# Kernel optimization log

Measured on AMD Instinct MI355X. Metric: run time of the kernel, lower is better.

The kernel has to match this reference:

```python
import jax, jax.numpy as jnp
import numpy as np
from jax import lax

T, D, HID, C = 16384, 1024, 1024, 16
H = HID // 2  # per-direction hidden size


def _uniform(key, shape, bound):
    return jax.random.uniform(key, shape, jnp.float32, -bound, bound)


def setup_inputs() -> dict:
    key = jax.random.key(0)
    ks = jax.random.split(key, 16)
    s = 1.0 / np.sqrt(H)        # PyTorch LSTM init bound
    sl = 1.0 / np.sqrt(HID)     # PyTorch Linear init bound
    return {
        "sequence": jax.random.normal(ks[0], (T, D), jnp.float32),
        "h0": jax.random.normal(ks[1], (2, 1, H), jnp.float32),
        "c0": jax.random.normal(ks[2], (2, 1, H), jnp.float32),
        "w_ih_f": _uniform(ks[3], (4 * H, D), s),
        "w_hh_f": _uniform(ks[4], (4 * H, H), s),
        "b_ih_f": _uniform(ks[5], (4 * H,), s),
        "b_hh_f": _uniform(ks[6], (4 * H,), s),
        "w_ih_b": _uniform(ks[7], (4 * H, D), s),
        "w_hh_b": _uniform(ks[8], (4 * H, H), s),
        "b_ih_b": _uniform(ks[9], (4 * H,), s),
        "b_hh_b": _uniform(ks[10], (4 * H,), s),
        "w_lin": _uniform(ks[11], (C, HID), sl),
        "b_lin": _uniform(ks[12], (C,), sl),
        "transitions": jax.random.uniform(ks[13], (C, C), jnp.float32),  # torch.rand
    }


def _lstm_scan(x, h0, c0, w_ih, w_hh, b_ih, b_hh, reverse):
    # x: [T, D]; PyTorch gate order: i, f, g, o
    def step(carry, xt):
        h, c = carry
        g = w_ih @ xt + b_ih + w_hh @ h + b_hh  # [4H]
        i, f, gg, o = jnp.split(g, 4)
        i = jax.nn.sigmoid(i)
        f = jax.nn.sigmoid(f)
        gg = jnp.tanh(gg)
        o = jax.nn.sigmoid(o)
        c = f * c + i * gg
        h = o * jnp.tanh(c)
        return (h, c), h
    _, hs = lax.scan(step, (h0, c0), x, reverse=reverse)
    return hs  # [T, H], hs[t] = hidden at time t (aligned for both directions)


def _viterbi(feats, transitions):
    # feats: [T, C]; init forward_var = zeros (per the original torch.full(..., 0))
    def vstep(fv, feat):
        scores = fv[None, :] + transitions          # [C_next, C_prev]
        bp = jnp.argmax(scores, axis=1)             # backpointers
        fv2 = jnp.max(scores, axis=1) + feat
        return fv2, bp
    fv, bps = lax.scan(vstep, jnp.zeros((C,), feats.dtype), feats)
    best = jnp.argmax(fv)
    path_score = fv[best]
    def bstep(b, bp_row):
        nb = bp_row[b]
        return nb, nb
    _, rev = lax.scan(bstep, best, bps, reverse=True)  # rev[t] = state before step t's transition
    best_path = jnp.concatenate([rev, best[None]])     # length T+1, matches torch output
    return path_score, best_path


def reference(sequence, h0, c0, w_ih_f, w_hh_f, b_ih_f, b_hh_f,
              w_ih_b, w_hh_b, b_ih_b, b_hh_b, w_lin, b_lin, transitions):
    hs_f = _lstm_scan(sequence, h0[0, 0], c0[0, 0], w_ih_f, w_hh_f, b_ih_f, b_hh_f, False)
    hs_b = _lstm_scan(sequence, h0[1, 0], c0[1, 0], w_ih_b, w_hh_b, b_ih_b, b_hh_b, True)
    lstm_out = jnp.concatenate([hs_f, hs_b], axis=-1)   # [T, HID]
    feats = lstm_out @ w_lin.T + b_lin                  # [T, C]
    return _viterbi(feats, transitions)
```

## Files before the change

kernel.cpp:

```cpp
#include <hip/hip_runtime.h>

#define T_STEPS 16384
#define TC      8192
#define DMODEL  1024
#define HID     512
#define G4      2048
#define NC      16

static const unsigned long long OFF_ZF    = 0ull;
static const unsigned long long OFF_ZB    = 16777216ull;
static const unsigned long long OFF_HF    = 33554432ull;
static const unsigned long long OFF_HB    = 41943040ull;
static const unsigned long long OFF_FEATS = 50331648ull;
static const unsigned long long OFF_CST   = 50593792ull;
static const unsigned long long FLOATS_TOTAL = 50594816ull;
static const unsigned long long OFF_BP_B = FLOATS_TOTAL * 4ull;
static const unsigned long long OFF_P_B  = OFF_BP_B + 262144ull;
static const unsigned long long OFF_EX_B = OFF_P_B + 262144ull;
static const unsigned long long OFF_BT_B = OFF_EX_B + 16384ull;
static const unsigned long long NEED_B   = OFF_BT_B + 64ull;

__global__ __launch_bounds__(256) void zgemm_kernel(
    const float* __restrict__ X,
    const float* __restrict__ W0, const float* __restrict__ bi0,
    const float* __restrict__ bh0, float* __restrict__ Z0, int t00,
    const float* __restrict__ W1, const float* __restrict__ bi1,
    const float* __restrict__ bh1, float* __restrict__ Z1, int t01)
{
    const int dir = blockIdx.z;
    const float* W  = dir ? W1 : W0;
    const float* bi = dir ? bi1 : bi0;
    const float* bh = dir ? bh1 : bh0;
    float* Z        = dir ? Z1 : Z0;
    const int t0    = dir ? t01 : t00;

    const int m0 = blockIdx.y * 64;
    const int n0 = blockIdx.x * 64;

    __shared__ __align__(16) float As[16][68];
    __shared__ __align__(16) float Bs[16][68];

    const int tid = threadIdx.x;
    const int lr = tid >> 2;
    const int ls = tid & 3;
    const int tx = tid & 15;
    const int ty = tid >> 4;

    float acc[4][4] = {};

    for (int k0 = 0; k0 < DMODEL; k0 += 16) {
        float4 av = *(const float4*)&X[(unsigned long long)(t0 + m0 + lr) * DMODEL + k0 + ls * 4];
        float4 bv = *(const float4*)&W[(unsigned long long)(n0 + lr) * DMODEL + k0 + ls * 4];
        __syncthreads();
        As[ls*4+0][lr] = av.x; As[ls*4+1][lr] = av.y; As[ls*4+2][lr] = av.z; As[ls*4+3][lr] = av.w;
        Bs[ls*4+0][lr] = bv.x; Bs[ls*4+1][lr] = bv.y; Bs[ls*4+2][lr] = bv.z; Bs[ls*4+3][lr] = bv.w;
        __syncthreads();
        #pragma unroll
        for (int k = 0; k < 16; ++k) {
            float4 a = *(const float4*)&As[k][ty * 4];
            float4 b = *(const float4*)&Bs[k][tx * 4];
            acc[0][0] += a.x*b.x; acc[0][1] += a.x*b.y; acc[0][2] += a.x*b.z; acc[0][3] += a.x*b.w;
            acc[1][0] += a.y*b.x; acc[1][1] += a.y*b.y; acc[1][2] += a.y*b.z; acc[1][3] += a.y*b.w;
            acc[2][0] += a.z*b.x; acc[2][1] += a.z*b.y; acc[2][2] += a.z*b.z; acc[2][3] += a.z*b.w;
            acc[3][0] += a.w*b.x; acc[3][1] += a.w*b.y; acc[3][2] += a.w*b.z; acc[3][3] += a.w*b.w;
        }
    }
    float4 bi4 = *(const float4*)&bi[n0 + tx * 4];
    float4 bh4 = *(const float4*)&bh[n0 + tx * 4];
    float bx = bi4.x + bh4.x, by = bi4.y + bh4.y, bz = bi4.z + bh4.z, bw = bi4.w + bh4.w;
    #pragma unroll
    for (int i = 0; i < 4; ++i) {
        float4 o;
        o.x = acc[i][0] + bx; o.y = acc[i][1] + by; o.z = acc[i][2] + bz; o.w = acc[i][3] + bw;
        *(float4*)&Z[(unsigned long long)(m0 + ty * 4 + i) * G4 + n0 + tx * 4] = o;
    }
}

__global__ __launch_bounds__(256, 1) void recur_kernel(
    const float* __restrict__ Zf, const float* __restrict__ Zb,
    const float* __restrict__ whh_f, const float* __restrict__ whh_b,
    const float* __restrict__ h0, const float* __restrict__ c0,
    float* __restrict__ hf, float* __restrict__ hb,
    unsigned long long* __restrict__ exf, unsigned long long* __restrict__ exb,
    float* __restrict__ c_state, int s0, int zf_t0, int zb_t0)
{
    const int wg  = blockIdx.x;
    const int dir = wg >> 5;
    const int g   = wg & 31;
    const float* Z   = dir ? Zb : Zf;
    const float* whh = dir ? whh_b : whh_f;
    float* hout      = dir ? hb : hf;
    const int zt0    = dir ? zb_t0 : zf_t0;
    unsigned long long* ex = dir ? exb : exf;

    const int tid  = threadIdx.x;
    const int w    = tid >> 6;
    const int lane = tid & 63;
    const int G    = lane >> 4;
    const int u    = lane & 15;
    const int R    = 512 * G + 16 * g + u;

    float wreg[128];
    {
        const float* src = &whh[(unsigned long long)R * HID + w * 128];
        #pragma unroll
        for (int j4 = 0; j4 < 32; ++j4) {
            float4 v = *(const float4*)&src[j4 * 4];
            wreg[j4*4+0] = v.x; wreg[j4*4+1] = v.y; wreg[j4*4+2] = v.z; wreg[j4*4+3] = v.w;
        }
    }

    __shared__ __align__(16) float h_lds[512];
    __shared__ __align__(16) float p_lds[256];

    float cst = 0.0f;
    if (w == 0 && lane < 16)
        cst = (s0 == 0) ? c0[dir * HID + 16 * g + lane]
                        : c_state[dir * HID + 16 * g + lane];

    for (int s = s0; s < s0 + TC; ++s) {
        const int t = dir ? (T_STEPS - 1 - s) : s;
        float zr = 0.0f;
        if (w == 0) zr = Z[(unsigned long long)(t - zt0) * G4 + R];

        int dead = 0;
        if (s == 0) {
            h_lds[2*tid]   = h0[dir * HID + 2*tid];
            h_lds[2*tid+1] = h0[dir * HID + 2*tid + 1];
        } else {
            const int par = s & 1;
            const unsigned long long want = (unsigned long long)s;
            #pragma unroll
            for (int r = 0; r < 2; ++r) {
                const int idx = 2 * tid + r;
                unsigned long long v;
                int guard = 0;
                do {
                    v = __hip_atomic_load(&ex[par * 512 + idx], __ATOMIC_RELAXED,
                                          __HIP_MEMORY_SCOPE_AGENT);
                    if (++guard >= (1 << 17)) { dead = 1; break; }
                } while ((v >> 32) != want);
                union { unsigned int ui; float f; } cv;
                cv.ui = (unsigned int)v;
                h_lds[idx] = cv.f;
            }
        }
        if (__syncthreads_or(dead)) break;

        float acc = 0.0f;
        const float4* h4 = (const float4*)&h_lds[w * 128];
        #pragma unroll
        for (int c4 = 0; c4 < 32; ++c4) {
            float4 hv = h4[c4];
            acc += wreg[c4*4+0]*hv.x + wreg[c4*4+1]*hv.y
                 + wreg[c4*4+2]*hv.z + wreg[c4*4+3]*hv.w;
        }
        p_lds[tid] = acc;
        __syncthreads();

        if (w == 0) {
            float rv = p_lds[lane] + p_lds[64+lane] + p_lds[128+lane] + p_lds[192+lane] + zr;
            float iv = __shfl(rv, u,      64);
            float fv = __shfl(rv, u + 16, 64);
            float gv = __shfl(rv, u + 32, 64);
            float ov = __shfl(rv, u + 48, 64);
            if (lane < 16) {
                float ig = 1.0f / (1.0f + expf(-iv));
                float fg = 1.0f / (1.0f + expf(-fv));
                float gg = tanhf(gv);
                float og = 1.0f / (1.0f + expf(-ov));
                float cn = fg * cst + ig * gg;
                float hn = og * tanhf(cn);
                cst = cn;
                hout[(unsigned long long)t * HID + 16 * g + lane] = hn;
                union { float f; unsigned int ui; } cv; cv.f = hn;
                unsigned long long pv = ((unsigned long long)(s + 1) << 32) | (unsigned long long)cv.ui;
                __hip_atomic_store(&ex[((s + 1) & 1) * 512 + 16 * g + lane], pv,
                                   __ATOMIC_RELAXED, __HIP_MEMORY_SCOPE_AGENT);
            }
        }
        __syncthreads();
    }

    if (w == 0 && lane < 16)
        c_state[dir * HID + 16 * g + lane] = cst;
}

__global__ __launch_bounds__(256) void feats_kernel(
    const float* __restrict__ hf, const float* __restrict__ hb,
    const float* __restrict__ wlin, const float* __restrict__ blin,
    float* __restrict__ feats)
{
    const int t = blockIdx.x;
    __shared__ __align__(16) float hl[1024];
    const int tid = threadIdx.x;
    {
        const float* src = (tid < 128) ? &hf[(unsigned long long)t * HID + tid * 4]
                                       : &hb[(unsigned long long)t * HID + (tid - 128) * 4];
        *(float4*)&hl[tid * 4] = *(const float4*)src;
    }
    __syncthreads();
    const int c = tid >> 4, p = tid & 15;
    float s = 0.0f;
    #pragma unroll
    for (int j = 0; j < 16; ++j) {
        float4 h4 = *(const float4*)&hl[p * 4 + j * 64];
        float4 w4 = *(const float4*)&wlin[(unsigned long long)c * 1024 + p * 4 + j * 64];
        s += h4.x*w4.x + h4.y*w4.y + h4.z*w4.z + h4.w*w4.w;
    }
    s += __shfl_down(s, 8, 16);
    s += __shfl_down(s, 4, 16);
    s += __shfl_down(s, 2, 16);
    s += __shfl_down(s, 1, 16);
    if (p == 0) feats[t * NC + c] = s + blin[c];
}

__global__ __launch_bounds__(64) void viterbi_kernel(
    const float* __restrict__ feats, const float* __restrict__ trans,
    unsigned char* __restrict__ bp, float* __restrict__ out,
    unsigned int* __restrict__ bT)
{
    __shared__ __align__(16) float fl[4096];
    __shared__ __align__(16) float fvs[16];
    const int l = threadIdx.x;
    float tr[16];
    if (l < 16) {
        #pragma unroll
        for (int j = 0; j < 16; ++j) tr[j] = trans[l * 16 + j];
    }
    float fv = 0.0f;
    for (int cb = 0; cb < 64; ++cb) {
        #pragma unroll
        for (int j = 0; j < 16; ++j)
            *(float4*)&fl[j * 256 + l * 4] =
                *(const float4*)&feats[cb * 4096 + j * 256 + l * 4];
        __syncthreads();
        if (l < 16) {
            for (int k = 0; k < 256; ++k) {
                float m = __shfl(fv, 0, 16) + tr[0];
                int bi = 0;
                #pragma unroll
                for (int j = 1; j < 16; ++j) {
                    float sc = __shfl(fv, j, 16) + tr[j];
                    if (sc > m) { m = sc; bi = j; }
                }
                bp[(unsigned long long)(cb * 256 + k) * 16 + l] = (unsigned char)bi;
                fv = m + fl[k * 16 + l];
            }
        }
        __syncthreads();
    }
    if (l < 16) fvs[l] = fv;
    __syncthreads();
    if (l == 0) {
        float best = fvs[0]; int bi = 0;
        #pragma unroll
        for (int j = 1; j < 16; ++j) if (fvs[j] > best) { best = fvs[j]; bi = j; }
        out[0] = best;
        out[1 + T_STEPS] = (float)bi;
        *bT = (unsigned int)bi;
    }
}

__global__ __launch_bounds__(64) void maps_kernel(
    const unsigned char* __restrict__ bp, unsigned char* __restrict__ P)
{
    const int j = blockIdx.x;
    const int l = threadIdx.x;
    __shared__ __align__(16) unsigned char lb[4096];
    __shared__ __align__(16) unsigned char lp[4096];
    #pragma unroll
    for (int i = 0; i < 4; ++i)
        *(uint4*)&lb[i * 1024 + l * 16] = *(const uint4*)&bp[(unsigned long long)j * 4096 + i * 1024 + l * 16];
    __syncthreads();
    if (l < 16) {
        int cur = l;
        for (int k = 255; k >= 0; --k) {
            cur = lb[k * 16 + cur];
            lp[k * 16 + l] = (unsigned char)cur;
        }
    }
    __syncthreads();
    #pragma unroll
    for (int i = 0; i < 4; ++i)
        *(uint4*)&P[(unsigned long long)j * 4096 + i * 1024 + l * 16] = *(const uint4*)&lp[i * 1024 + l * 16];
}

__global__ __launch_bounds__(64) void path_kernel(
    const unsigned char* __restrict__ P, const unsigned int* __restrict__ bT,
    float* __restrict__ out)
{
    const int j = blockIdx.x;
    const int l = threadIdx.x;
    int e = (int)(*bT);
    for (int i = 63; i > j; --i) e = P[(unsigned long long)i * 4096 + e];
    for (int k = l; k < 256; k += 64)
        out[1 + j * 256 + k] = (float)P[(unsigned long long)j * 4096 + k * 16 + e];
}

__global__ void fb_kernel(float* out, int n, float v0) {
    int i = blockIdx.x * 256 + threadIdx.x;
    if (i < n) out[i] = (i == 0) ? v0 : 0.0f;
}

extern "C" void kernel_launch(void* const* d_in, const int* in_sizes, int n_in,
                              void* d_out, int out_size, void* d_ws, size_t ws_size,
                              hipStream_t stream) {
    const float* seq   = (const float*)d_in[0];
    const float* h0    = (const float*)d_in[1];
    const float* c0    = (const float*)d_in[2];
    const float* wih_f = (const float*)d_in[3];
    const float* whh_f = (const float*)d_in[4];
    const float* bih_f = (const float*)d_in[5];
    const float* bhh_f = (const float*)d_in[6];
    const float* wih_b = (const float*)d_in[7];
    const float* whh_b = (const float*)d_in[8];
    const float* bih_b = (const float*)d_in[9];
    const float* bhh_b = (const float*)d_in[10];
    const float* wlin  = (const float*)d_in[11];
    const float* blin  = (const float*)d_in[12];
    const float* trans = (const float*)d_in[13];
    float* out = (float*)d_out;

    if (ws_size < NEED_B) {
        fb_kernel<<<(out_size + 255) / 256, 256, 0, stream>>>(out, out_size, -(float)ws_size);
        return;
    }

    float* wsf = (float*)d_ws;
    float* Zf    = wsf + OFF_ZF;
    float* Zb    = wsf + OFF_ZB;
    float* hf    = wsf + OFF_HF;
    float* hb    = wsf + OFF_HB;
    float* feats = wsf + OFF_FEATS;
    float* cstate= wsf + OFF_CST;
    unsigned char* bp = (unsigned char*)d_ws + OFF_BP_B;
    unsigned char* P  = (unsigned char*)d_ws + OFF_P_B;
    unsigned long long* exf = (unsigned long long*)((char*)d_ws + OFF_EX_B);
    unsigned long long* exb = exf + 1024;
    unsigned int* bT = (unsigned int*)((char*)d_ws + OFF_BT_B);

    hipMemsetAsync((void*)exf, 0, 16384, stream);

    for (int ci = 0; ci < 2; ++ci) {
        int s0    = ci * TC;
        int zf_t0 = ci * TC;
        int zb_t0 = T_STEPS - (ci + 1) * TC;

        zgemm_kernel<<<dim3(32, TC / 64, 2), 256, 0, stream>>>(
            seq, wih_f, bih_f, bhh_f, Zf, zf_t0, wih_b, bih_b, bhh_b, Zb, zb_t0);

        void* args[] = { (void*)&Zf, (void*)&Zb, (void*)&whh_f, (void*)&whh_b,
                         (void*)&h0, (void*)&c0, (void*)&hf, (void*)&hb,
                         (void*)&exf, (void*)&exb, (void*)&cstate,
                         (void*)&s0, (void*)&zf_t0, (void*)&zb_t0 };
        hipError_t e = hipLaunchCooperativeKernel(
            reinterpret_cast<void*>(recur_kernel), dim3(64), dim3(256),
            args, 0, stream);
        if (e != hipSuccess) {
            recur_kernel<<<64, 256, 0, stream>>>(Zf, Zb, whh_f, whh_b, h0, c0,
                                                 hf, hb, exf, exb, cstate,
                                                 s0, zf_t0, zb_t0);
        }
    }

    feats_kernel<<<16384, 256, 0, stream>>>(hf, hb, wlin, blin, feats);
    viterbi_kernel<<<1, 64, 0, stream>>>(feats, trans, bp, out, bT);
    maps_kernel<<<64, 64, 0, stream>>>(bp, P);
    path_kernel<<<64, 64, 0, stream>>>(P, bT, out);
}
```

Baseline: 47.75 ms.

## Fuse input-projection GEMM and LSTM recurrence into one persistent producer-consumer kernel

Merges the input-projection GEMM and the recurrent LSTM kernel into one cooperative launch of 256 blocks. 64 blocks run the recurrence while 192 blocks compute Z in 1024-step chunks into a double buffer, with counters signalling when each chunk is ready or consumed. This hides the GEMM time behind the latency-bound recurrence and shrinks the Z workspace. The recurrence also double-buffers the partial-sum LDS to drop one barrier per step and computes the gate activations across all 64 lanes before the shuffles. The risks are contention between GEMM blocks and recurrence blocks for memory bandwidth, and spin-wait deadlocks that are only escaped through guard counters.

```diff
diff --git a/kernel.cpp b/kernel.cpp
--- a/kernel.cpp
+++ b/kernel.cpp
@@ -1,189 +1,214 @@
 #include <hip/hip_runtime.h>
 
 #define T_STEPS 16384
-#define TC      8192
+#define CSTEPS  1024
+#define NCHUNK  16
 #define DMODEL  1024
 #define HID     512
 #define G4      2048
 #define NC      16
-
-static const unsigned long long OFF_ZF    = 0ull;
-static const unsigned long long OFF_ZB    = 16777216ull;
-static const unsigned long long OFF_HF    = 33554432ull;
-static const unsigned long long OFF_HB    = 41943040ull;
-static const unsigned long long OFF_FEATS = 50331648ull;
-static const unsigned long long OFF_CST   = 50593792ull;
-static const unsigned long long FLOATS_TOTAL = 50594816ull;
-static const unsigned long long OFF_BP_B = FLOATS_TOTAL * 4ull;
-static const unsigned long long OFF_P_B  = OFF_BP_B + 262144ull;
-static const unsigned long long OFF_EX_B = OFF_P_B + 262144ull;
-static const unsigned long long OFF_BT_B = OFF_EX_B + 16384ull;
-static const unsigned long long NEED_B   = OFF_BT_B + 64ull;
-
-__global__ __launch_bounds__(256) void zgemm_kernel(
-    const float* __restrict__ X,
-    const float* __restrict__ W0, const float* __restrict__ bi0,
-    const float* __restrict__ bh0, float* __restrict__ Z0, int t00,
-    const float* __restrict__ W1, const float* __restrict__ bi1,
-    const float* __restrict__ bh1, float* __restrict__ Z1, int t01)
-{
-    const int dir = blockIdx.z;
-    const float* W  = dir ? W1 : W0;
-    const float* bi = dir ? bi1 : bi0;
-    const float* bh = dir ? bh1 : bh0;
-    float* Z        = dir ? Z1 : Z0;
-    const int t0    = dir ? t01 : t00;
-
-    const int m0 = blockIdx.y * 64;
-    const int n0 = blockIdx.x * 64;
-
-    __shared__ __align__(16) float As[16][68];
-    __shared__ __align__(16) float Bs[16][68];
-
-    const int tid = threadIdx.x;
-    const int lr = tid >> 2;
-    const int ls = tid & 3;
-    const int tx = tid & 15;
-    const int ty = tid >> 4;
-
-    float acc[4][4] = {};
-
-    for (int k0 = 0; k0 < DMODEL; k0 += 16) {
-        float4 av = *(const float4*)&X[(unsigned long long)(t0 + m0 + lr) * DMODEL + k0 + ls * 4];
-        float4 bv = *(const float4*)&W[(unsigned long long)(n0 + lr) * DMODEL + k0 + ls * 4];
-        __syncthreads();
-        As[ls*4+0][lr] = av.x; As[ls*4+1][lr] = av.y; As[ls*4+2][lr] = av.z; As[ls*4+3][lr] = av.w;
-        Bs[ls*4+0][lr] = bv.x; Bs[ls*4+1][lr] = bv.y; Bs[ls*4+2][lr] = bv.z; Bs[ls*4+3][lr] = bv.w;
-        __syncthreads();
-        #pragma unroll
-        for (int k = 0; k < 16; ++k) {
-            float4 a = *(const float4*)&As[k][ty * 4];
-            float4 b = *(const float4*)&Bs[k][tx * 4];
-            acc[0][0] += a.x*b.x; acc[0][1] += a.x*b.y; acc[0][2] += a.x*b.z; acc[0][3] += a.x*b.w;
-            acc[1][0] += a.y*b.x; acc[1][1] += a.y*b.y; acc[1][2] += a.y*b.z; acc[1][3] += a.y*b.w;
-            acc[2][0] += a.z*b.x; acc[2][1] += a.z*b.y; acc[2][2] += a.z*b.z; acc[2][3] += a.z*b.w;
-            acc[3][0] += a.w*b.x; acc[3][1] += a.w*b.y; acc[3][2] += a.w*b.z; acc[3][3] += a.w*b.w;
-        }
-    }
-    float4 bi4 = *(const float4*)&bi[n0 + tx * 4];
-    float4 bh4 = *(const float4*)&bh[n0 + tx * 4];
-    float bx = bi4.x + bh4.x, by = bi4.y + bh4.y, bz = bi4.z + bh4.z, bw = bi4.w + bh4.w;
-    #pragma unroll
-    for (int i = 0; i < 4; ++i) {
-        float4 o;
-        o.x = acc[i][0] + bx; o.y = acc[i][1] + by; o.z = acc[i][2] + bz; o.w = acc[i][3] + bw;
-        *(float4*)&Z[(unsigned long long)(m0 + ty * 4 + i) * G4 + n0 + tx * 4] = o;
-    }
-}
-
-__global__ __launch_bounds__(256, 1) void recur_kernel(
-    const float* __restrict__ Zf, const float* __restrict__ Zb,
+#define NGEMMB  192
+
+static const size_t OFF_Z     = 0;
+static const size_t OFF_HF    = 8388608ull;
+static const size_t OFF_HB    = 16777216ull;
+static const size_t OFF_FEATS = 25165824ull;
+static const size_t FLOATS_TOTAL = 25427968ull;
+static const size_t OFF_BP_B  = FLOATS_TOTAL * 4ull;
+static const size_t OFF_P_B   = OFF_BP_B + 262144ull;
+static const size_t OFF_EX_B  = OFF_P_B + 262144ull;
+static const size_t OFF_CTR_B = OFF_EX_B + 16384ull;
+static const size_t NEED_B    = OFF_CTR_B + 256ull;
+
+__global__ __launch_bounds__(256, 1) void fused_kernel(
+    const float* __restrict__ seq,
+    const float* __restrict__ wih_f, const float* __restrict__ bih_f, const float* __restrict__ bhh_f,
+    const float* __restrict__ wih_b, const float* __restrict__ bih_b, const float* __restrict__ bhh_b,
     const float* __restrict__ whh_f, const float* __restrict__ whh_b,
     const float* __restrict__ h0, const float* __restrict__ c0,
     float* __restrict__ hf, float* __restrict__ hb,
+    float* __restrict__ Zbuf,
     unsigned long long* __restrict__ exf, unsigned long long* __restrict__ exb,
-    float* __restrict__ c_state, int s0, int zf_t0, int zb_t0)
-{
-    const int wg  = blockIdx.x;
-    const int dir = wg >> 5;
-    const int g   = wg & 31;
-    const float* Z   = dir ? Zb : Zf;
-    const float* whh = dir ? whh_b : whh_f;
-    float* hout      = dir ? hb : hf;
-    const int zt0    = dir ? zb_t0 : zf_t0;
-    unsigned long long* ex = dir ? exb : exf;
-
-    const int tid  = threadIdx.x;
-    const int w    = tid >> 6;
-    const int lane = tid & 63;
-    const int G    = lane >> 4;
-    const int u    = lane & 15;
-    const int R    = 512 * G + 16 * g + u;
-
-    float wreg[128];
-    {
-        const float* src = &whh[(unsigned long long)R * HID + w * 128];
-        #pragma unroll
-        for (int j4 = 0; j4 < 32; ++j4) {
-            float4 v = *(const float4*)&src[j4 * 4];
-            wreg[j4*4+0] = v.x; wreg[j4*4+1] = v.y; wreg[j4*4+2] = v.z; wreg[j4*4+3] = v.w;
-        }
-    }
-
-    __shared__ __align__(16) float h_lds[512];
-    __shared__ __align__(16) float p_lds[256];
-
-    float cst = 0.0f;
-    if (w == 0 && lane < 16)
-        cst = (s0 == 0) ? c0[dir * HID + 16 * g + lane]
-                        : c_state[dir * HID + 16 * g + lane];
-
-    for (int s = s0; s < s0 + TC; ++s) {
-        const int t = dir ? (T_STEPS - 1 - s) : s;
-        float zr = 0.0f;
-        if (w == 0) zr = Z[(unsigned long long)(t - zt0) * G4 + R];
+    unsigned int* __restrict__ gemm_done, unsigned int* __restrict__ recur_prog)
+{
+    const int bid = blockIdx.x;
+    const int tid = threadIdx.x;
+
+    if (bid < 64) {
+        const int dir = bid >> 5;
+        const int g   = bid & 31;
+        const float* whh = dir ? whh_b : whh_f;
+        float* hout      = dir ? hb : hf;
+        unsigned long long* ex = dir ? exb : exf;
+
+        const int w = tid >> 6, lane = tid & 63;
+        const int G = lane >> 4, u = lane & 15;
+        const int R = 512 * G + 16 * g + u;
+
+        float wreg[128];
+        {
+            const float* src = &whh[(size_t)R * HID + w * 128];
+            #pragma unroll
+            for (int j = 0; j < 32; ++j) {
+                float4 v = *(const float4*)&src[j * 4];
+                wreg[j*4+0]=v.x; wreg[j*4+1]=v.y; wreg[j*4+2]=v.z; wreg[j*4+3]=v.w;
+            }
+        }
+
+        __shared__ __align__(16) float h_lds[512];
+        __shared__ __align__(16) float p_lds[2][256];
+
+        float cst = 0.f;
+        if (w == 0 && lane < 16) cst = c0[dir * HID + 16 * g + lane];
+
+        {
+            const int i0 = 128 * w + 2 * lane;
+            h_lds[i0]     = h0[dir * HID + i0];
+            h_lds[i0 + 1] = h0[dir * HID + i0 + 1];
+        }
 
         int dead = 0;
-        if (s == 0) {
-            h_lds[2*tid]   = h0[dir * HID + 2*tid];
-            h_lds[2*tid+1] = h0[dir * HID + 2*tid + 1];
-        } else {
+        const float* Zd = Zbuf + (size_t)dir * 2 * CSTEPS * G4;
+
+        for (int s = 0; s < T_STEPS; ++s) {
+            if ((s & (CSTEPS - 1)) == 0) {
+                if (tid == 0) {
+                    const int cg = s >> 10;
+                    int guard = 0; unsigned int gd;
+                    do {
+                        gd = __hip_atomic_load(&gemm_done[cg], __ATOMIC_RELAXED,
+                                               __HIP_MEMORY_SCOPE_AGENT);
+                        if (++guard > (1 << 20)) { dead = 1; break; }
+                    } while (gd < (unsigned)NGEMMB);
+                }
+                if (__syncthreads_or(dead)) break;
+            }
+            const int c   = s >> 10;
             const int par = s & 1;
-            const unsigned long long want = (unsigned long long)s;
-            #pragma unroll
-            for (int r = 0; r < 2; ++r) {
-                const int idx = 2 * tid + r;
-                unsigned long long v;
+            const int t   = dir ? (T_STEPS - 1 - s) : s;
+            const int rr  = dir ? (1023 - (s & 1023)) : (s & 1023);
+
+            float zr = 0.f;
+            if (w == 0)
+                zr = __hip_atomic_load(&Zd[((size_t)(c & 1) * CSTEPS + rr) * G4 + R],
+                                       __ATOMIC_RELAXED, __HIP_MEMORY_SCOPE_AGENT);
+
+            if (s > 0) {
+                const unsigned long long want = (unsigned long long)(unsigned)s;
+                const int i0 = 128 * w + 2 * lane;
+                unsigned long long v0, v1;
                 int guard = 0;
+                for (;;) {
+                    v0 = __hip_atomic_load(&ex[par*512 + i0],     __ATOMIC_RELAXED, __HIP_MEMORY_SCOPE_AGENT);
+                    v1 = __hip_atomic_load(&ex[par*512 + i0 + 1], __ATOMIC_RELAXED, __HIP_MEMORY_SCOPE_AGENT);
+                    if (((v0 >> 32) == want) & ((v1 >> 32) == want)) break;
+                    if (++guard > (1 << 16)) { dead = 1; break; }
+                }
+                union { unsigned int ui; float f; } ca, cb;
+                ca.ui = (unsigned int)v0; cb.ui = (unsigned int)v1;
+                h_lds[i0]     = ca.f;
+                h_lds[i0 + 1] = cb.f;
+            }
+
+            float acc = 0.f;
+            {
+                const float4* h4 = (const float4*)&h_lds[w * 128];
+                #pragma unroll
+                for (int j = 0; j < 32; ++j) {
+                    float4 hv = h4[j];
+                    acc += wreg[j*4+0]*hv.x + wreg[j*4+1]*hv.y
+                         + wreg[j*4+2]*hv.z + wreg[j*4+3]*hv.w;
+                }
+            }
+            p_lds[par][tid] = acc;
+            if (__syncthreads_or(dead)) break;
+
+            if (w == 0) {
+                float rv = p_lds[par][lane] + p_lds[par][64+lane]
+                         + p_lds[par][128+lane] + p_lds[par][192+lane] + zr;
+                float a = (G == 2) ? tanhf(rv) : 1.f / (1.f + expf(-rv));
+                float ig = __shfl(a, u,      64);
+                float fg = __shfl(a, u + 16, 64);
+                float gg = __shfl(a, u + 32, 64);
+                float og = __shfl(a, u + 48, 64);
+                if (lane < 16) {
+                    float cn = fg * cst + ig * gg;
+                    cst = cn;
+                    float hn = og * tanhf(cn);
+                    union { float f; unsigned int ui; } cv; cv.f = hn;
+                    __hip_atomic_store(&ex[((s + 1) & 1) * 512 + 16 * g + lane],
+                        ((unsigned long long)(unsigned)(s + 1) << 32) | (unsigned long long)cv.ui,
+                        __ATOMIC_RELAXED, __HIP_MEMORY_SCOPE_AGENT);
+                    hout[(size_t)t * HID + 16 * g + lane] = hn;
+                }
+                if ((s & (CSTEPS - 1)) == (CSTEPS - 1) && lane == 0)
+                    __hip_atomic_fetch_add(&recur_prog[c], 1u, __ATOMIC_RELAXED,
+                                           __HIP_MEMORY_SCOPE_AGENT);
+            }
+        }
+    } else {
+        const int gb = bid - 64;
+        __shared__ __align__(16) float As[16][68];
+        __shared__ __align__(16) float Bs[16][68];
+        const int lr = tid >> 2, ls = tid & 3, tx = tid & 15, ty = tid >> 4;
+
+        for (int cc = 0; cc < NCHUNK; ++cc) {
+            if (cc >= 2 && tid == 0) {
+                int guard = 0; unsigned int rp;
                 do {
-                    v = __hip_atomic_load(&ex[par * 512 + idx], __ATOMIC_RELAXED,
-                                          __HIP_MEMORY_SCOPE_AGENT);
-                    if (++guard >= (1 << 17)) { dead = 1; break; }
-                } while ((v >> 32) != want);
-                union { unsigned int ui; float f; } cv;
-                cv.ui = (unsigned int)v;
-                h_lds[idx] = cv.f;
-            }
-        }
-        if (__syncthreads_or(dead)) break;
-
-        float acc = 0.0f;
-        const float4* h4 = (const float4*)&h_lds[w * 128];
-        #pragma unroll
-        for (int c4 = 0; c4 < 32; ++c4) {
-            float4 hv = h4[c4];
-            acc += wreg[c4*4+0]*hv.x + wreg[c4*4+1]*hv.y
-                 + wreg[c4*4+2]*hv.z + wreg[c4*4+3]*hv.w;
-        }
-        p_lds[tid] = acc;
-        __syncthreads();
-
-        if (w == 0) {
-            float rv = p_lds[lane] + p_lds[64+lane] + p_lds[128+lane] + p_lds[192+lane] + zr;
-            float iv = __shfl(rv, u,      64);
-            float fv = __shfl(rv, u + 16, 64);
-            float gv = __shfl(rv, u + 32, 64);
-            float ov = __shfl(rv, u + 48, 64);
-            if (lane < 16) {
-                float ig = 1.0f / (1.0f + expf(-iv));
-                float fg = 1.0f / (1.0f + expf(-fv));
-                float gg = tanhf(gv);
-                float og = 1.0f / (1.0f + expf(-ov));
-                float cn = fg * cst + ig * gg;
-                float hn = og * tanhf(cn);
-                cst = cn;
-                hout[(unsigned long long)t * HID + 16 * g + lane] = hn;
-                union { float f; unsigned int ui; } cv; cv.f = hn;
-                unsigned long long pv = ((unsigned long long)(s + 1) << 32) | (unsigned long long)cv.ui;
-                __hip_atomic_store(&ex[((s + 1) & 1) * 512 + 16 * g + lane], pv,
-                                   __ATOMIC_RELAXED, __HIP_MEMORY_SCOPE_AGENT);
-            }
-        }
-        __syncthreads();
-    }
-
-    if (w == 0 && lane < 16)
-        c_state[dir * HID + 16 * g + lane] = cst;
+                    rp = __hip_atomic_load(&recur_prog[cc - 2], __ATOMIC_RELAXED,
+                                           __HIP_MEMORY_SCOPE_AGENT);
+                    if (++guard > (1 << 20)) break;
+                } while (rp < 64u);
+            }
+            __syncthreads();
+
+            for (int tix = gb; tix < 2 * 16 * 32; tix += NGEMMB) {
+                const int dr  = tix >> 9;
+                const int rem = tix & 511;
+                const int mt  = rem >> 5;
+                const int nt  = rem & 31;
+                const int t0  = dr ? (T_STEPS - (cc + 1) * CSTEPS) : (cc * CSTEPS);
+                const float* W  = dr ? wih_b : wih_f;
+                const float* bi = dr ? bih_b : bih_f;
+                const float* bh = dr ? bhh_b : bhh_f;
+                float* Zt = Zbuf + (size_t)(dr * 2 + (cc & 1)) * CSTEPS * G4;
+
+                float acc[4][4] = {};
+                for (int k0 = 0; k0 < DMODEL; k0 += 16) {
+                    float4 av = *(const float4*)&seq[(size_t)(t0 + mt*64 + lr) * DMODEL + k0 + ls*4];
+                    float4 bv = *(const float4*)&W[(size_t)(nt*64 + lr) * DMODEL + k0 + ls*4];
+                    __syncthreads();
+                    As[ls*4+0][lr]=av.x; As[ls*4+1][lr]=av.y; As[ls*4+2][lr]=av.z; As[ls*4+3][lr]=av.w;
+                    Bs[ls*4+0][lr]=bv.x; Bs[ls*4+1][lr]=bv.y; Bs[ls*4+2][lr]=bv.z; Bs[ls*4+3][lr]=bv.w;
+                    __syncthreads();
+                    #pragma unroll
+                    for (int k = 0; k < 16; ++k) {
+                        float4 a = *(const float4*)&As[k][ty * 4];
+                        float4 b = *(const float4*)&Bs[k][tx * 4];
+                        acc[0][0]+=a.x*b.x; acc[0][1]+=a.x*b.y; acc[0][2]+=a.x*b.z; acc[0][3]+=a.x*b.w;
+                        acc[1][0]+=a.y*b.x; acc[1][1]+=a.y*b.y; acc[1][2]+=a.y*b.z; acc[1][3]+=a.y*b.w;
+                        acc[2][0]+=a.z*b.x; acc[2][1]+=a.z*b.y; acc[2][2]+=a.z*b.z; acc[2][3]+=a.z*b.w;
+                        acc[3][0]+=a.w*b.x; acc[3][1]+=a.w*b.y; acc[3][2]+=a.w*b.z; acc[3][3]+=a.w*b.w;
+                    }
+                }
+                float4 b4  = *(const float4*)&bi[nt * 64 + tx * 4];
+                float4 c4v = *(const float4*)&bh[nt * 64 + tx * 4];
+                float bx=b4.x+c4v.x, by=b4.y+c4v.y, bz=b4.z+c4v.z, bw_=b4.w+c4v.w;
+                #pragma unroll
+                for (int i = 0; i < 4; ++i) {
+                    float4 o;
+                    o.x=acc[i][0]+bx; o.y=acc[i][1]+by; o.z=acc[i][2]+bz; o.w=acc[i][3]+bw_;
+                    *(float4*)&Zt[(size_t)(mt*64 + ty*4 + i) * G4 + nt*64 + tx*4] = o;
+                }
+            }
+            __threadfence();
+            __syncthreads();
+            if (tid == 0)
+                __hip_atomic_fetch_add(&gemm_done[cc], 1u, __ATOMIC_RELEASE,
+                                       __HIP_MEMORY_SCOPE_AGENT);
+        }
+    }
 }
 
 __global__ __launch_bounds__(256) void feats_kernel(
@@ -195,8 +220,8 @@
     __shared__ __align__(16) float hl[1024];
     const int tid = threadIdx.x;
     {
-        const float* src = (tid < 128) ? &hf[(unsigned long long)t * HID + tid * 4]
-                                       : &hb[(unsigned long long)t * HID + (tid - 128) * 4];
+        const float* src = (tid < 128) ? &hf[(size_t)t * HID + tid * 4]
+                                       : &hb[(size_t)t * HID + (tid - 128) * 4];
         *(float4*)&hl[tid * 4] = *(const float4*)src;
     }
     __syncthreads();
@@ -205,7 +230,7 @@
     #pragma unroll
     for (int j = 0; j < 16; ++j) {
         float4 h4 = *(const float4*)&hl[p * 4 + j * 64];
-        float4 w4 = *(const float4*)&wlin[(unsigned long long)c * 1024 + p * 4 + j * 64];
+        float4 w4 = *(const float4*)&wlin[(size_t)c * 1024 + p * 4 + j * 64];
         s += h4.x*w4.x + h4.y*w4.y + h4.z*w4.z + h4.w*w4.w;
     }
     s += __shfl_down(s, 8, 16);
@@ -244,7 +269,7 @@
                     float sc = __shfl(fv, j, 16) + tr[j];
                     if (sc > m) { m = sc; bi = j; }
                 }
-                bp[(unsigned long long)(cb * 256 + k) * 16 + l] = (unsigned char)bi;
+                bp[(size_t)(cb * 256 + k) * 16 + l] = (unsigned char)bi;
                 fv = m + fl[k * 16 + l];
             }
         }
@@ -271,7 +296,7 @@
     __shared__ __align__(16) unsigned char lp[4096];
     #pragma unroll
     for (int i = 0; i < 4; ++i)
-        *(uint4*)&lb[i * 1024 + l * 16] = *(const uint4*)&bp[(unsigned long long)j * 4096 + i * 1024 + l * 16];
+        *(uint4*)&lb[i * 1024 + l * 16] = *(const uint4*)&bp[(size_t)j * 4096 + i * 1024 + l * 16];
     __syncthreads();
     if (l < 16) {
         int cur = l;
@@ -283,7 +308,7 @@
     __syncthreads();
     #pragma unroll
     for (int i = 0; i < 4; ++i)
-        *(uint4*)&P[(unsigned long long)j * 4096 + i * 1024 + l * 16] = *(const uint4*)&lp[i * 1024 + l * 16];
+        *(uint4*)&P[(size_t)j * 4096 + i * 1024 + l * 16] = *(const uint4*)&lp[i * 1024 + l * 16];
 }
 
 __global__ __launch_bounds__(64) void path_kernel(
@@ -293,9 +318,9 @@
     const int j = blockIdx.x;
     const int l = threadIdx.x;
     int e = (int)(*bT);
-    for (int i = 63; i > j; --i) e = P[(unsigned long long)i * 4096 + e];
+    for (int i = 63; i > j; --i) e = P[(size_t)i * 4096 + e];
     for (int k = l; k < 256; k += 64)
-        out[1 + j * 256 + k] = (float)P[(unsigned long long)j * 4096 + k * 16 + e];
+        out[1 + j * 256 + k] = (float)P[(size_t)j * 4096 + k * 16 + e];
 }
 
 __global__ void fb_kernel(float* out, int n, float v0) {
@@ -328,39 +353,38 @@
     }
 
     float* wsf = (float*)d_ws;
-    float* Zf    = wsf + OFF_ZF;
-    float* Zb    = wsf + OFF_ZB;
+    float* Zbuf  = wsf + OFF_Z;
     float* hf    = wsf + OFF_HF;
     float* hb    = wsf + OFF_HB;
     float* feats = wsf + OFF_FEATS;
-    float* cstate= wsf + OFF_CST;
     unsigned char* bp = (unsigned char*)d_ws + OFF_BP_B;
     unsigned char* P  = (unsigned char*)d_ws + OFF_P_B;
     unsigned long long* exf = (unsigned long long*)((char*)d_ws + OFF_EX_B);
     unsigned long long* exb = exf + 1024;
-    unsigned int* bT = (unsigned int*)((char*)d_ws + OFF_BT_B);
-
-    hipMemsetAsync((void*)exf, 0, 16384, stream);
-
-    for (int ci = 0; ci < 2; ++ci) {
-        int s0    = ci * TC;
-        int zf_t0 = ci * TC;
-        int zb_t0 = T_STEPS - (ci + 1) * TC;
-
-        zgemm_kernel<<<dim3(32, TC / 64, 2), 256, 0, stream>>>(
-            seq, wih_f, bih_f, bhh_f, Zf, zf_t0, wih_b, bih_b, bhh_b, Zb, zb_t0);
-
-        void* args[] = { (void*)&Zf, (void*)&Zb, (void*)&whh_f, (void*)&whh_b,
-                         (void*)&h0, (void*)&c0, (void*)&hf, (void*)&hb,
-                         (void*)&exf, (void*)&exb, (void*)&cstate,
-                         (void*)&s0, (void*)&zf_t0, (void*)&zb_t0 };
+    unsigned int* ctr = (unsigned int*)((char*)d_ws + OFF_CTR_B);
+    unsigned int* gemm_done  = ctr;
+    unsigned int* recur_prog = ctr + 16;
+    unsigned int* bT         = ctr + 32;
+
+    hipMemsetAsync((void*)exf, 0, 16384 + 256, stream);
+
+    {
+        void* args[] = { (void*)&seq,
+                         (void*)&wih_f, (void*)&bih_f, (void*)&bhh_f,
+                         (void*)&wih_b, (void*)&bih_b, (void*)&bhh_b,
+                         (void*)&whh_f, (void*)&whh_b,
+                         (void*)&h0, (void*)&c0,
+                         (void*)&hf, (void*)&hb, (void*)&Zbuf,
+                         (void*)&exf, (void*)&exb,
+                         (void*)&gemm_done, (void*)&recur_prog };
         hipError_t e = hipLaunchCooperativeKernel(
-            reinterpret_cast<void*>(recur_kernel), dim3(64), dim3(256),
+            reinterpret_cast<void*>(fused_kernel), dim3(256), dim3(256),
             args, 0, stream);
         if (e != hipSuccess) {
-            recur_kernel<<<64, 256, 0, stream>>>(Zf, Zb, whh_f, whh_b, h0, c0,
-                                                 hf, hb, exf, exb, cstate,
-                                                 s0, zf_t0, zb_t0);
+            fused_kernel<<<256, 256, 0, stream>>>(
+                seq, wih_f, bih_f, bhh_f, wih_b, bih_b, bhh_b,
+                whh_f, whh_b, h0, c0, hf, hb, Zbuf, exf, exb,
+                gemm_done, recur_prog);
         }
     }
 
```

After: 43.74 ms. 8.4% less time.
